# Kernel tuning notes

Hardware: AMD Instinct MI355X
Metric: run time of the kernel (lower is better)

## Reference

```python
import jax, jax.numpy as jnp
import numpy as np

NUM_CLASSES = 10
BATCH = 2048
DIM = 128
TEMPERATURE = 0.07
BASE_TEMPERATURE = 0.07


def setup_inputs() -> dict:
    key = jax.random.key(0)
    k1, k2 = jax.random.split(key)
    preds = jax.random.normal(k1, (NUM_CLASSES, BATCH, DIM), dtype=jnp.float32)
    target = jax.random.randint(k2, (BATCH,), 0, NUM_CLASSES, dtype=jnp.int64)
    log_vars = jnp.zeros((NUM_CLASSES,), dtype=jnp.float32)
    return {"preds": preds, "target": target, "log_vars": log_vars}


def _per_class_loss(features, labels_bin):
    # features: [B, D], labels_bin: [B] in {0,1} (target == class i)
    B = features.shape[0]
    mask = (labels_bin[:, None] == labels_bin[None, :]).astype(features.dtype)  # [B,B]
    logits_mask = 1.0 - jnp.eye(B, dtype=features.dtype)                        # zero diagonal
    sim = jnp.matmul(features, features.T) / TEMPERATURE                        # [B,B]
    norms = jnp.linalg.norm(features, axis=1, keepdims=True)                    # [B,1]
    logits = sim / (norms * norms.T)                                            # cosine / temp
    mask = mask * logits_mask
    exp_logits = jnp.exp(logits) * logits_mask
    log_prob = logits - jnp.log(exp_logits.sum(axis=1, keepdims=True))
    mean_log_prob_pos = (mask * log_prob).sum(axis=1) / mask.sum(axis=1)
    loss = -(TEMPERATURE / BASE_TEMPERATURE) * mean_log_prob_pos
    return loss.mean()


def reference(preds, target, log_vars):
    # labels_bin[i] = (target == i), one row per class
    labels_bin = (target[None, :] == jnp.arange(NUM_CLASSES, dtype=target.dtype)[:, None])
    losses = jax.vmap(_per_class_loss)(preds, labels_bin)  # [num_classes]
    final_loss = jnp.sum(jnp.exp(-log_vars) * losses + log_vars)
    return final_loss
```

## Files before the change

### kernel.cpp

```cpp
#include <hip/hip_runtime.h>
#include <hip/hip_bf16.h>
#include <math.h>

#define NUM_CLASSES 10
#define BATCH 2048
#define DIM 128
#define INV_T 14.285714285714286f
#define NTILE 16
#define NPAIR 136
#define LROW 72

typedef __attribute__((ext_vector_type(8))) short bf16x8;
typedef __attribute__((ext_vector_type(4))) float f32x4;

__global__ __launch_bounds__(256) void normalize_kernel(
    const float* __restrict__ preds, __hip_bfloat16* __restrict__ g,
    float* __restrict__ zero_buf)
{
    int b = blockIdx.x;
    int t = threadIdx.x;
    if (t < 8) zero_buf[b * 8 + t] = 0.0f;

    int row  = b * 4 + (t >> 6);
    int lane = t & 63;
    const float2* src = (const float2*)(preds + (size_t)row * DIM);
    float2 v = src[lane];
    float ss = v.x * v.x + v.y * v.y;
#pragma unroll
    for (int m = 32; m; m >>= 1) ss += __shfl_xor(ss, m, 64);
    float rn = 1.0f / sqrtf(ss);
    __hip_bfloat162 o;
    o.x = __float2bfloat16(v.x * rn);
    o.y = __float2bfloat16(v.y * rn);
    *(__hip_bfloat162*)(g + (size_t)row * DIM + lane * 2) = o;
}

__global__ __launch_bounds__(256) void gram_kernel(
    const __hip_bfloat16* __restrict__ g, const int* __restrict__ target,
    float* __restrict__ denom, float* __restrict__ s2)
{
    int p = blockIdx.x;
    int by = 0, rem = NTILE;
    while (p >= rem) { p -= rem; --rem; ++by; }
    const int bx   = by + p;
    const int cls  = blockIdx.y;
    const int row0 = by * 128;
    const int col0 = bx * 128;
    const bool isDiag = (by == bx);
    const __hip_bfloat16* gc = g + (size_t)cls * BATCH * DIM;

    __shared__ __align__(16) ushort smem[2 * 128 * LROW];
    ushort* As = smem;
    ushort* Bs = smem + 128 * LROW;

    const int t    = threadIdx.x;
    const int wid  = t >> 6;
    const int lane = t & 63;
    const int tx   = lane & 15;
    const int quad = lane >> 4;
    const int wm   = (wid >> 1) * 64;
    const int wn   = (wid & 1) * 64;

    f32x4 acc[4][4] = {};

    for (int kt = 0; kt < 2; ++kt) {
#pragma unroll
        for (int s = 0; s < 4; ++s) {
            int q = t + s * 256;
            int r = q >> 3;
            int c = q & 7;
            float4 va = *(const float4*)(gc + (size_t)(row0 + r) * DIM + kt * 64 + c * 8);
            *(float4*)(&As[r * LROW + c * 8]) = va;
            if (!isDiag) {
                float4 vb = *(const float4*)(gc + (size_t)(col0 + r) * DIM + kt * 64 + c * 8);
                *(float4*)(&Bs[r * LROW + c * 8]) = vb;
            }
        }
        __syncthreads();

        const ushort* BsR = isDiag ? As : Bs;
#pragma unroll
        for (int ks = 0; ks < 2; ++ks) {
            bf16x8 af[4], bg[4];
#pragma unroll
            for (int i = 0; i < 4; ++i) {
                af[i] = *(const bf16x8*)(&As [(wm + i * 16 + tx) * LROW + ks * 32 + quad * 8]);
                bg[i] = *(const bf16x8*)(&BsR[(wn + i * 16 + tx) * LROW + ks * 32 + quad * 8]);
            }
#pragma unroll
            for (int i = 0; i < 4; ++i)
#pragma unroll
                for (int j = 0; j < 4; ++j)
                    acc[i][j] = __builtin_amdgcn_mfma_f32_16x16x32_bf16(
                        af[i], bg[j], acc[i][j], 0, 0, 0);
        }
        __syncthreads();
    }

    unsigned laMask = 0;
#pragma unroll
    for (int i = 0; i < 4; ++i)
#pragma unroll
        for (int r = 0; r < 4; ++r)
            if (target[row0 + wm + i * 16 + quad * 4 + r] == cls)
                laMask |= 1u << (i * 4 + r);
    int lb[4];
#pragma unroll
    for (int j = 0; j < 4; ++j) lb[j] = (target[col0 + wn + j * 16 + tx] == cls);

    float2* rbuf = (float2*)smem;
    float2 pcol[4] = {};

#pragma unroll
    for (int i = 0; i < 4; ++i) {
        float2 prow[4] = {};
#pragma unroll
        for (int j = 0; j < 4; ++j) {
            int cg = col0 + wn + j * 16 + tx;
            int lbj = lb[j];
#pragma unroll
            for (int r = 0; r < 4; ++r) {
                int rg = row0 + wm + i * 16 + quad * 4 + r;
                float logit = acc[i][j][r] * INV_T;
                float e = __expf(logit);
                bool dg = isDiag && (cg == rg);
                e = dg ? 0.0f : e;
                bool same = (((laMask >> (i * 4 + r)) & 1) == (unsigned)lbj) && !dg;
                float sl = same ? logit : 0.0f;
                prow[r].x += e; prow[r].y += sl;
                pcol[j].x += e; pcol[j].y += sl;
            }
        }
#pragma unroll
        for (int r = 0; r < 4; ++r)
            rbuf[wid * 1088 + (i * 16 + quad * 4 + r) * 17 + tx] = prow[r];
    }
    __syncthreads();

    if (t < 128) {
        int rl = t & 63, grp = t >> 6;
        float den = 0.0f, sp = 0.0f;
#pragma unroll
        for (int w = 0; w < 2; ++w) {
            int base = (2 * grp + w) * 1088 + rl * 17;
#pragma unroll
            for (int x = 0; x < 16; ++x) {
                float2 v = rbuf[base + x];
                den += v.x; sp += v.y;
            }
        }
        atomicAdd(&denom[cls * BATCH + row0 + t], den);
        atomicAdd(&s2   [cls * BATCH + row0 + t], sp);
    }

    if (!isDiag) {
        __syncthreads();
        float2* cbuf = (float2*)smem;
#pragma unroll
        for (int j = 0; j < 4; ++j)
            cbuf[wid * 320 + (j * 16 + tx) * 5 + quad] = pcol[j];
        __syncthreads();
        if (t < 128) {
            int cl = t & 63, grp = t >> 6;
            float den = 0.0f, sp = 0.0f;
#pragma unroll
            for (int w = 0; w < 2; ++w) {
                int base = (grp + 2 * w) * 320 + cl * 5;
#pragma unroll
                for (int q = 0; q < 4; ++q) {
                    float2 v = cbuf[base + q];
                    den += v.x; sp += v.y;
                }
            }
            atomicAdd(&denom[cls * BATCH + col0 + t], den);
            atomicAdd(&s2   [cls * BATCH + col0 + t], sp);
        }
    }
}

__global__ __launch_bounds__(1024) void final_kernel(
    const float* __restrict__ denom, const float* __restrict__ s2,
    const int* __restrict__ target, const float* __restrict__ log_vars,
    float* __restrict__ out)
{
    __shared__ int counts[NUM_CLASSES];
    __shared__ float wsum[16];
    int t = threadIdx.x;
    if (t < NUM_CLASSES) counts[t] = 0;
    __syncthreads();
    for (int i = t; i < BATCH; i += 1024) atomicAdd(&counts[target[i]], 1);
    __syncthreads();

    float partial = 0.0f;
    for (int idx = t; idx < NUM_CLASSES * BATCH; idx += 1024) {
        int i = idx >> 11;
        int a = idx & (BATCH - 1);
        int cnt = (target[a] == i) ? (counts[i] - 1) : (BATCH - counts[i] - 1);
        float mlpp = s2[idx] / (float)cnt - logf(denom[idx]);
        partial += __expf(-log_vars[i]) * mlpp;
    }
#pragma unroll
    for (int m = 32; m; m >>= 1) partial += __shfl_xor(partial, m, 64);
    if ((t & 63) == 0) wsum[t >> 6] = partial;
    __syncthreads();
    if (t == 0) {
        float tot = 0.0f;
        for (int w = 0; w < 16; ++w) tot += wsum[w];
        float lvsum = 0.0f;
        for (int i = 0; i < NUM_CLASSES; ++i) lvsum += log_vars[i];
        out[0] = -tot / (float)BATCH + lvsum;
    }
}

extern "C" void kernel_launch(void* const* d_in, const int* in_sizes, int n_in,
                              void* d_out, int out_size, void* d_ws, size_t ws_size,
                              hipStream_t stream)
{
    const float* preds    = (const float*)d_in[0];
    const int*   target   = (const int*)  d_in[1];
    const float* log_vars = (const float*)d_in[2];
    float* out = (float*)d_out;

    __hip_bfloat16* gbf = (__hip_bfloat16*)d_ws;
    float* denom = (float*)((char*)d_ws + (size_t)NUM_CLASSES * BATCH * DIM * 2);
    float* s2    = denom + (size_t)NUM_CLASSES * BATCH;

    normalize_kernel<<<NUM_CLASSES * BATCH / 4, 256, 0, stream>>>(preds, gbf, denom);
    gram_kernel<<<dim3(NPAIR, NUM_CLASSES), 256, 0, stream>>>(gbf, target, denom, s2);
    final_kernel<<<1, 1024, 0, stream>>>(denom, s2, target, log_vars, out);
}
```

Baseline: 99.10 us.

## Load gram tiles directly to LDS with XOR swizzle and merge row/column reductions

```diff
diff --git a/kernel.cpp b/kernel.cpp
--- a/kernel.cpp
+++ b/kernel.cpp
@@ -8,10 +8,16 @@
 #define INV_T 14.285714285714286f
 #define NTILE 16
 #define NPAIR 136
-#define LROW 72
 
 typedef __attribute__((ext_vector_type(8))) short bf16x8;
 typedef __attribute__((ext_vector_type(4))) float f32x4;
+
+__device__ __forceinline__ void load_lds16(const void* g, void* lds) {
+    __builtin_amdgcn_global_load_lds(
+        (const __attribute__((address_space(1))) unsigned int*)g,
+        (__attribute__((address_space(3))) unsigned int*)lds,
+        16, 0, 0);
+}
 
 __global__ __launch_bounds__(256) void normalize_kernel(
     const float* __restrict__ preds, __hip_bfloat16* __restrict__ g,
@@ -47,11 +53,11 @@
     const int row0 = by * 128;
     const int col0 = bx * 128;
     const bool isDiag = (by == bx);
-    const __hip_bfloat16* gc = g + (size_t)cls * BATCH * DIM;
-
-    __shared__ __align__(16) ushort smem[2 * 128 * LROW];
+    const ushort* gc = (const ushort*)g + (size_t)cls * BATCH * DIM;
+
+    __shared__ __align__(16) ushort smem[2 * 128 * 128];
     ushort* As = smem;
-    ushort* Bs = smem + 128 * LROW;
+    ushort* Bs = smem + 128 * 128;
 
     const int t    = threadIdx.x;
     const int wid  = t >> 6;
@@ -61,41 +67,38 @@
     const int wm   = (wid >> 1) * 64;
     const int wn   = (wid & 1) * 64;
 
+    const int lr = lane >> 4;
+    const int lp = lane & 15;
+#pragma unroll
+    for (int s = 0; s < 8; ++s) {
+        int rb = s * 16 + wid * 4;
+        int r  = rb + lr;
+        int c  = lp ^ (r & 15);
+        load_lds16(gc + (size_t)(row0 + r) * DIM + c * 8, &As[rb * 128]);
+        if (!isDiag)
+            load_lds16(gc + (size_t)(col0 + r) * DIM + c * 8, &Bs[rb * 128]);
+    }
+    __syncthreads();
+
+    const ushort* BsR = isDiag ? As : Bs;
     f32x4 acc[4][4] = {};
-
-    for (int kt = 0; kt < 2; ++kt) {
-#pragma unroll
-        for (int s = 0; s < 4; ++s) {
-            int q = t + s * 256;
-            int r = q >> 3;
-            int c = q & 7;
-            float4 va = *(const float4*)(gc + (size_t)(row0 + r) * DIM + kt * 64 + c * 8);
-            *(float4*)(&As[r * LROW + c * 8]) = va;
-            if (!isDiag) {
-                float4 vb = *(const float4*)(gc + (size_t)(col0 + r) * DIM + kt * 64 + c * 8);
-                *(float4*)(&Bs[r * LROW + c * 8]) = vb;
-            }
-        }
-        __syncthreads();
-
-        const ushort* BsR = isDiag ? As : Bs;
-#pragma unroll
-        for (int ks = 0; ks < 2; ++ks) {
-            bf16x8 af[4], bg[4];
-#pragma unroll
-            for (int i = 0; i < 4; ++i) {
-                af[i] = *(const bf16x8*)(&As [(wm + i * 16 + tx) * LROW + ks * 32 + quad * 8]);
-                bg[i] = *(const bf16x8*)(&BsR[(wn + i * 16 + tx) * LROW + ks * 32 + quad * 8]);
-            }
-#pragma unroll
-            for (int i = 0; i < 4; ++i)
-#pragma unroll
-                for (int j = 0; j < 4; ++j)
-                    acc[i][j] = __builtin_amdgcn_mfma_f32_16x16x32_bf16(
-                        af[i], bg[j], acc[i][j], 0, 0, 0);
-        }
-        __syncthreads();
-    }
+#pragma unroll
+    for (int ks = 0; ks < 4; ++ks) {
+        bf16x8 af[4], bg[4];
+#pragma unroll
+        for (int i = 0; i < 4; ++i) {
+            int pa = ((ks * 4 + quad) ^ tx) * 8;
+            af[i] = *(const bf16x8*)&As [(wm + i * 16 + tx) * 128 + pa];
+            bg[i] = *(const bf16x8*)&BsR[(wn + i * 16 + tx) * 128 + pa];
+        }
+#pragma unroll
+        for (int i = 0; i < 4; ++i)
+#pragma unroll
+            for (int j = 0; j < 4; ++j)
+                acc[i][j] = __builtin_amdgcn_mfma_f32_16x16x32_bf16(
+                    af[i], bg[j], acc[i][j], 0, 0, 0);
+    }
+    __syncthreads();
 
     unsigned laMask = 0;
 #pragma unroll
@@ -109,6 +112,7 @@
     for (int j = 0; j < 4; ++j) lb[j] = (target[col0 + wn + j * 16 + tx] == cls);
 
     float2* rbuf = (float2*)smem;
+    float2* cbuf = (float2*)(smem + 17408);
     float2 pcol[4] = {};
 
 #pragma unroll
@@ -135,6 +139,9 @@
         for (int r = 0; r < 4; ++r)
             rbuf[wid * 1088 + (i * 16 + quad * 4 + r) * 17 + tx] = prow[r];
     }
+#pragma unroll
+    for (int j = 0; j < 4; ++j)
+        cbuf[wid * 320 + (j * 16 + tx) * 5 + quad] = pcol[j];
     __syncthreads();
 
     if (t < 128) {
@@ -151,30 +158,21 @@
         }
         atomicAdd(&denom[cls * BATCH + row0 + t], den);
         atomicAdd(&s2   [cls * BATCH + row0 + t], sp);
-    }
-
-    if (!isDiag) {
-        __syncthreads();
-        float2* cbuf = (float2*)smem;
-#pragma unroll
-        for (int j = 0; j < 4; ++j)
-            cbuf[wid * 320 + (j * 16 + tx) * 5 + quad] = pcol[j];
-        __syncthreads();
-        if (t < 128) {
-            int cl = t & 63, grp = t >> 6;
-            float den = 0.0f, sp = 0.0f;
-#pragma unroll
-            for (int w = 0; w < 2; ++w) {
-                int base = (grp + 2 * w) * 320 + cl * 5;
-#pragma unroll
-                for (int q = 0; q < 4; ++q) {
-                    float2 v = cbuf[base + q];
-                    den += v.x; sp += v.y;
-                }
+    } else if (!isDiag) {
+        int u = t - 128;
+        int cl = u & 63, grp = u >> 6;
+        float den = 0.0f, sp = 0.0f;
+#pragma unroll
+        for (int w = 0; w < 2; ++w) {
+            int base = (grp + 2 * w) * 320 + cl * 5;
+#pragma unroll
+            for (int q = 0; q < 4; ++q) {
+                float2 v = cbuf[base + q];
+                den += v.x; sp += v.y;
             }
-            atomicAdd(&denom[cls * BATCH + col0 + t], den);
-            atomicAdd(&s2   [cls * BATCH + col0 + t], sp);
-        }
+        }
+        atomicAdd(&denom[cls * BATCH + col0 + u], den);
+        atomicAdd(&s2   [cls * BATCH + col0 + u], sp);
     }
 }
 
```

Measured after the change: 91.88 us. 7.3% less time.
